# Kernel optimization log

Hardware: AMD Instinct MI355X
Metric: run time of the kernel (lower is better)

Reference implementation:

```python
import jax, jax.numpy as jnp
from jax import lax
import numpy as np

SEQ_LEN, BATCH, HIDDEN, VOCAB = 256, 32, 512, 1024


def setup_inputs() -> dict:
    key = jax.random.key(0)
    k1, k2, k3, k4, k5 = jax.random.split(key, 5)
    enc_outs = jax.random.normal(k1, (SEQ_LEN, BATCH, HIDDEN), dtype=jnp.float32)
    W = jax.random.normal(k2, (VOCAB, HIDDEN), dtype=jnp.float32) * (1.0 / np.sqrt(HIDDEN))
    b = jnp.zeros((VOCAB,), dtype=jnp.float32)
    transition = jax.random.normal(k3, (VOCAB, VOCAB), dtype=jnp.float32) * 0.05
    targets = jax.random.randint(k4, (SEQ_LEN, BATCH), 0, VOCAB, dtype=jnp.int32)
    lengths = jax.random.randint(k5, (BATCH,), 1, SEQ_LEN + 1, dtype=jnp.int32)
    return {"enc_outs": enc_outs, "W": W, "b": b, "transition": transition,
            "targets": targets, "lengths": lengths}


def _crf_loss(enc_outs, W, b, transition, targets, lengths):
    # logits: [T, B, V]
    logits = jnp.einsum('tbh,vh->tbv', enc_outs, W) + b
    T, B, V = logits.shape
    # mask[t, b] = 1 if t < lengths[b]
    mask = (jnp.arange(T)[:, None] < lengths[None, :]).astype(logits.dtype)  # [T, B]

    # ---- partition function: forward algorithm as a scan over time ----
    def step(Z, inp):
        logit_t, mask_t = inp  # [B, V], [B]
        # scores[b, i, j] = Z[b, i] + transition[i, j] + emit[b, j]
        Z_t = jax.nn.logsumexp(Z[:, :, None] + transition[None, :, :] + logit_t[:, None, :], axis=1)
        Z = jnp.where(mask_t[:, None] > 0, Z_t, Z)
        return Z, None

    Z0 = logits[0]  # [B, V]
    Z, _ = lax.scan(step, Z0, (logits[1:], mask[1:]))
    log_Z = jax.nn.logsumexp(Z, axis=1)  # [B]

    # ---- gold path score ----
    emit = jnp.take_along_axis(logits, targets[:, :, None].astype(jnp.int32), axis=2)[:, :, 0]  # [T, B]
    emit_score = jnp.sum(emit * mask, axis=0)  # [B]
    trans = transition[targets[:-1], targets[1:]]  # [T-1, B]
    trans_score = jnp.sum(trans * mask[1:], axis=0)  # [B]
    score = emit_score + trans_score

    return jnp.mean(log_Z - score)


def reference(enc_outs, W, b, transition, targets, lengths):
    return _crf_loss(enc_outs, W, b, transition, targets, lengths)
```

## Files before the change

### kernel.cpp

```cpp
#include <hip/hip_runtime.h>
#include <math.h>
#include <stdint.h>

#define TLEN 256
#define NB   32
#define HID  512
#define VOC  1024

typedef __attribute__((ext_vector_type(2))) _Float16 half2_t;
typedef __attribute__((ext_vector_type(2))) __fp16  pk16_t;
typedef __attribute__((ext_vector_type(8))) _Float16 v8h;
typedef __attribute__((ext_vector_type(4))) float    v4f;

__device__ __forceinline__ float zload(const float* p) {
    return __hip_atomic_load(p, __ATOMIC_RELAXED, __HIP_MEMORY_SCOPE_AGENT);
}
__device__ __forceinline__ float2 zload2(const float* p) {
    unsigned long long u = __hip_atomic_load((const unsigned long long*)p,
                                             __ATOMIC_RELAXED, __HIP_MEMORY_SCOPE_AGENT);
    union { unsigned long long u; float2 f; } c; c.u = u; return c.f;
}
__device__ __forceinline__ void zstore(float* p, float v) {
    __hip_atomic_store(p, v, __ATOMIC_RELAXED, __HIP_MEMORY_SCOPE_AGENT);
}
__device__ __forceinline__ uint32_t pack_pkrtz(float a, float b) {
    pk16_t h = __builtin_amdgcn_cvt_pkrtz(a, b);
    return __builtin_bit_cast(uint32_t, h);
}
__device__ __forceinline__ int udot4(uint32_t a, uint32_t b, int acc) {
#if __has_builtin(__builtin_amdgcn_udot4)
    return __builtin_amdgcn_udot4(a, b, acc, false);
#else
    return acc + (int)((a & 255u) * (b & 255u))
               + (int)(((a >> 8) & 255u) * ((b >> 8) & 255u))
               + (int)(((a >> 16) & 255u) * ((b >> 16) & 255u))
               + (int)((a >> 24) * (b >> 24));
#endif
}

__global__ __launch_bounds__(256) void gemm_mfma(
    const float* __restrict__ A, const float* __restrict__ W,
    const float* __restrict__ bias, float* __restrict__ C)
{
    const int K = HID, N = VOC;
    __shared__ _Float16 As[128][40];
    __shared__ _Float16 Ws[128][40];
    int tid  = threadIdx.x;
    int wv   = tid >> 6;
    int lane = tid & 63;
    int wy = wv >> 1, wx = wv & 1;
    int quad = lane >> 4, l16 = lane & 15;
    int row0 = blockIdx.y << 7;
    int col0 = blockIdx.x << 7;

    v4f acc[4][4] = {};

    int sr = tid >> 1;
    int sk = (tid & 1) << 4;
    const float* ap = A + (size_t)(row0 + sr) * K + sk;
    const float* wp = W + (size_t)(col0 + sr) * K + sk;

    float4 a0 = *(const float4*)(ap);
    float4 a1 = *(const float4*)(ap + 4);
    float4 a2 = *(const float4*)(ap + 8);
    float4 a3 = *(const float4*)(ap + 12);
    float4 w0 = *(const float4*)(wp);
    float4 w1 = *(const float4*)(wp + 4);
    float4 w2 = *(const float4*)(wp + 8);
    float4 w3 = *(const float4*)(wp + 12);

    for (int k0 = 0; k0 < K; k0 += 32) {
        __syncthreads();
        uint32_t* ad = (uint32_t*)&As[sr][sk];
        ad[0] = pack_pkrtz(a0.x, a0.y); ad[1] = pack_pkrtz(a0.z, a0.w);
        ad[2] = pack_pkrtz(a1.x, a1.y); ad[3] = pack_pkrtz(a1.z, a1.w);
        ad[4] = pack_pkrtz(a2.x, a2.y); ad[5] = pack_pkrtz(a2.z, a2.w);
        ad[6] = pack_pkrtz(a3.x, a3.y); ad[7] = pack_pkrtz(a3.z, a3.w);
        uint32_t* wd = (uint32_t*)&Ws[sr][sk];
        wd[0] = pack_pkrtz(w0.x, w0.y); wd[1] = pack_pkrtz(w0.z, w0.w);
        wd[2] = pack_pkrtz(w1.x, w1.y); wd[3] = pack_pkrtz(w1.z, w1.w);
        wd[4] = pack_pkrtz(w2.x, w2.y); wd[5] = pack_pkrtz(w2.z, w2.w);
        wd[6] = pack_pkrtz(w3.x, w3.y); wd[7] = pack_pkrtz(w3.z, w3.w);
        __syncthreads();
        if (k0 + 32 < K) {
            const float* apn = ap + k0 + 32;
            const float* wpn = wp + k0 + 32;
            a0 = *(const float4*)(apn);
            a1 = *(const float4*)(apn + 4);
            a2 = *(const float4*)(apn + 8);
            a3 = *(const float4*)(apn + 12);
            w0 = *(const float4*)(wpn);
            w1 = *(const float4*)(wpn + 4);
            w2 = *(const float4*)(wpn + 8);
            w3 = *(const float4*)(wpn + 12);
        }
        v8h af[4], bf[4];
        #pragma unroll
        for (int i = 0; i < 4; ++i)
            af[i] = *(const v8h*)&As[wy * 64 + i * 16 + l16][quad * 8];
        #pragma unroll
        for (int j = 0; j < 4; ++j)
            bf[j] = *(const v8h*)&Ws[wx * 64 + j * 16 + l16][quad * 8];
        #pragma unroll
        for (int i = 0; i < 4; ++i)
            #pragma unroll
            for (int j = 0; j < 4; ++j)
                acc[i][j] = __builtin_amdgcn_mfma_f32_16x16x32_f16(af[i], bf[j], acc[i][j], 0, 0, 0);
    }
    #pragma unroll
    for (int i = 0; i < 4; ++i) {
        #pragma unroll
        for (int j = 0; j < 4; ++j) {
            int ccol = col0 + wx * 64 + j * 16 + l16;
            float bb = bias[ccol];
            #pragma unroll
            for (int r = 0; r < 4; ++r) {
                int rrow = row0 + wy * 64 + i * 16 + quad * 4 + r;
                C[(size_t)rrow * N + ccol] = acc[i][j][r] + bb;
            }
        }
    }
}

__global__ __launch_bounds__(512) void crf_scan(
    const float* __restrict__ logits, float* __restrict__ Za, float* __restrict__ Zb,
    const float* __restrict__ trans, const int* __restrict__ lengths,
    unsigned int* __restrict__ cnt)
{
    __shared__ float Sred[8][64][3];
    __shared__ float Mred[8][2];
    int tid  = threadIdx.x;
    int w    = tid >> 6;
    int lane = tid & 63;
    int h    = lane >> 5;
    int li   = lane & 31;
    int bg   = blockIdx.x;
    int cc   = blockIdx.y;
    int b0   = bg * 2;

    int len2[2];
    len2[0] = lengths[b0];
    len2[1] = lengths[b0 + 1];
    int lmax = max(len2[0], len2[1]);

    int c = (cc << 6) + lane;

    uint32_t Ereg[32];
    {
        const float* tc = trans + c;
        #pragma unroll
        for (int j = 0; j < 32; ++j) {
            int v0 = (w << 7) + (j << 2);
            float e0 = __expf(tc[(size_t)(v0 + 0) << 10]) * 196.f;
            float e1 = __expf(tc[(size_t)(v0 + 1) << 10]) * 196.f;
            float e2 = __expf(tc[(size_t)(v0 + 2) << 10]) * 196.f;
            float e3 = __expf(tc[(size_t)(v0 + 3) << 10]) * 196.f;
            uint32_t q0 = (uint32_t)__float2uint_rn(fminf(e0, 255.f));
            uint32_t q1 = (uint32_t)__float2uint_rn(fminf(e1, 255.f));
            uint32_t q2 = (uint32_t)__float2uint_rn(fminf(e2, 255.f));
            uint32_t q3 = (uint32_t)__float2uint_rn(fminf(e3, 255.f));
            Ereg[j] = q0 | (q1 << 8) | (q2 << 16) | (q3 << 24);
        }
    }

    float finv = 0.f;
    if (tid < 128) {
        int b = b0 + w;
        finv = (1 < len2[w]) ? logits[(size_t)NB * VOC + (size_t)b * VOC + c]
                             : logits[(size_t)b * VOC + c];
    }

    unsigned int* cbg = &cnt[bg << 4];

    const float* src = logits;
    for (int t = 1; t < TLEN; ++t) {
        float* dst = (t & 1) ? Za : Zb;
        if (t >= lmax) {
            if (src != Za && tid < 128) {
                int b = b0 + w;
                Za[(size_t)b * VOC + c] = zload(&src[(size_t)b * VOC + c]);
            }
            return;
        }
        const float* zp = src + (size_t)(b0 + h) * VOC + (w << 7) + (li << 2);
        float2 za = zload2(zp);
        float2 zb = zload2(zp + 2);
        float m = fmaxf(fmaxf(za.x, za.y), fmaxf(zb.x, zb.y));
        #pragma unroll
        for (int off = 16; off; off >>= 1) m = fmaxf(m, __shfl_xor(m, off));
        if (li == 0) Mred[w][h] = m;
        uint32_t q0 = (uint32_t)__float2uint_rn(__expf(za.x - m) * 255.f);
        uint32_t q1 = (uint32_t)__float2uint_rn(__expf(za.y - m) * 255.f);
        uint32_t q2 = (uint32_t)__float2uint_rn(__expf(zb.x - m) * 255.f);
        uint32_t q3 = (uint32_t)__float2uint_rn(__expf(zb.y - m) * 255.f);
        uint32_t pp = q0 | (q1 << 8) | (q2 << 16) | (q3 << 24);

        int a0a = 0, a0b = 0, a1a = 0, a1b = 0;
        #pragma unroll
        for (int j = 0; j < 32; j += 2) {
            uint32_t s00 = (uint32_t)__builtin_amdgcn_readlane((int)pp, j);
            uint32_t s10 = (uint32_t)__builtin_amdgcn_readlane((int)pp, j + 32);
            uint32_t s01 = (uint32_t)__builtin_amdgcn_readlane((int)pp, j + 1);
            uint32_t s11 = (uint32_t)__builtin_amdgcn_readlane((int)pp, j + 33);
            a0a = udot4(Ereg[j], s00, a0a);
            a1a = udot4(Ereg[j], s10, a1a);
            a0b = udot4(Ereg[j + 1], s01, a0b);
            a1b = udot4(Ereg[j + 1], s11, a1b);
        }
        Sred[w][lane][0] = (float)(a0a + a0b);
        Sred[w][lane][1] = (float)(a1a + a1b);
        __syncthreads();

        if (tid < 128) {
            float M = Mred[0][w];
            #pragma unroll
            for (int ww = 1; ww < 8; ++ww) M = fmaxf(M, Mred[ww][w]);
            float S = 0.f;
            #pragma unroll
            for (int ww = 0; ww < 8; ++ww)
                S += __expf(Mred[ww][w] - M) * Sred[ww][lane][w];
            int b = b0 + w;
            float outv;
            if (t < len2[w]) outv = finv + M + __logf(S * (1.0f / (255.f * 196.f)));
            else             outv = finv;
            zstore(&dst[(size_t)b * VOC + c], outv);
            int tn = t + 1;
            if (tn < len2[w]) finv = logits[((size_t)tn * NB + b) * VOC + c];
            else              finv = outv;
        }

        __syncthreads();
        if (tid == 0) {
            unsigned int tgt = (unsigned int)(t << 4);
            unsigned int old = __hip_atomic_fetch_add(cbg, 1u, __ATOMIC_RELAXED,
                                                      __HIP_MEMORY_SCOPE_AGENT);
            if (old + 1u != tgt) {
                while (__hip_atomic_load(cbg, __ATOMIC_RELAXED,
                                         __HIP_MEMORY_SCOPE_AGENT) < tgt)
                    __builtin_amdgcn_s_sleep(1);
            }
        }
        __syncthreads();
        src = dst;
    }
}

__global__ __launch_bounds__(256) void crf_finish2(
    const float* __restrict__ Zfin, const float* __restrict__ logits,
    const float* __restrict__ trans, const int* __restrict__ targets,
    const int* __restrict__ lengths, float* __restrict__ out)
{
    __shared__ float redm[4], reds[4], reda[4];
    int b = blockIdx.x;
    int tid = threadIdx.x;
    int lane = tid & 63, wv = tid >> 6;
    const float* zr = Zfin + (size_t)b * VOC;

    float m = -1e30f;
    #pragma unroll
    for (int i = 0; i < 4; ++i) m = fmaxf(m, zr[tid + (i << 8)]);
    #pragma unroll
    for (int off = 32; off; off >>= 1) m = fmaxf(m, __shfl_xor(m, off));
    if (lane == 0) redm[wv] = m;
    __syncthreads();
    m = fmaxf(fmaxf(redm[0], redm[1]), fmaxf(redm[2], redm[3]));

    float s = 0.f;
    #pragma unroll
    for (int i = 0; i < 4; ++i) s += __expf(zr[tid + (i << 8)] - m);
    #pragma unroll
    for (int off = 32; off; off >>= 1) s += __shfl_xor(s, off);
    if (lane == 0) reds[wv] = s;

    int len = lengths[b];
    float acc = 0.f;
    int t = tid;
    if (t < len) {
        int tg = targets[t * NB + b];
        acc = logits[((size_t)t * NB + b) * VOC + tg];
        if (t >= 1) acc += trans[(size_t)targets[(t - 1) * NB + b] * VOC + tg];
    }
    #pragma unroll
    for (int off = 32; off; off >>= 1) acc += __shfl_xor(acc, off);
    if (lane == 0) reda[wv] = acc;
    __syncthreads();

    if (tid == 0) {
        float S = reds[0] + reds[1] + reds[2] + reds[3];
        float logZ = m + __logf(S);
        float score = reda[0] + reda[1] + reda[2] + reda[3];
        atomicAdd(out, (logZ - score) * (1.0f / NB));
    }
}

extern "C" void kernel_launch(void* const* d_in, const int* in_sizes, int n_in,
                              void* d_out, int out_size, void* d_ws, size_t ws_size,
                              hipStream_t stream)
{
    const float* enc   = (const float*)d_in[0];
    const float* W     = (const float*)d_in[1];
    const float* bias  = (const float*)d_in[2];
    const float* trans = (const float*)d_in[3];
    const int* targets = (const int*)d_in[4];
    const int* lengths = (const int*)d_in[5];
    float* out = (float*)d_out;

    float* ws     = (float*)d_ws;
    float* logits = ws;
    float* Za     = logits + (size_t)TLEN * NB * VOC;
    float* Zb     = Za + (size_t)NB * VOC;
    unsigned int* cnt = (unsigned int*)(Zb + (size_t)NB * VOC);

    (void)hipMemsetAsync(cnt, 0, 16 * 16 * sizeof(unsigned int), stream);
    (void)hipMemsetAsync(out, 0, sizeof(float), stream);
    gemm_mfma<<<dim3(VOC / 128, TLEN * NB / 128), 256, 0, stream>>>(enc, W, bias, logits);
    crf_scan<<<dim3(16, 16), 512, 0, stream>>>(logits, Za, Zb, trans, lengths, cnt);
    crf_finish2<<<NB, 256, 0, stream>>>(Za, logits, trans, targets, lengths, out);
}
```

Before: 606.6 us.

## Replace per-step global counter barrier with tagged data flags in scan

Removes the per-timestep atomic counter barrier across the 16 column blocks of each batch pair. Instead, each block embeds a step tag in the low 4 mantissa bits of every stored Z value and spins until the values it reads carry the expected tag. Shared reduction buffers are double-buffered by step parity, which lets the second __syncthreads per step go away. Final Z values are written to a separate Zfin buffer at each sequence's last step. The cost is lost low mantissa precision, polling on the data itself, and a memset of the Z buffers at launch.

```diff
diff --git a/kernel.cpp b/kernel.cpp
--- a/kernel.cpp
+++ b/kernel.cpp
@@ -7,14 +7,10 @@
 #define HID  512
 #define VOC  1024
 
-typedef __attribute__((ext_vector_type(2))) _Float16 half2_t;
 typedef __attribute__((ext_vector_type(2))) __fp16  pk16_t;
 typedef __attribute__((ext_vector_type(8))) _Float16 v8h;
 typedef __attribute__((ext_vector_type(4))) float    v4f;
 
-__device__ __forceinline__ float zload(const float* p) {
-    return __hip_atomic_load(p, __ATOMIC_RELAXED, __HIP_MEMORY_SCOPE_AGENT);
-}
 __device__ __forceinline__ float2 zload2(const float* p) {
     unsigned long long u = __hip_atomic_load((const unsigned long long*)p,
                                              __ATOMIC_RELAXED, __HIP_MEMORY_SCOPE_AGENT);
@@ -124,11 +120,11 @@
 
 __global__ __launch_bounds__(512) void crf_scan(
     const float* __restrict__ logits, float* __restrict__ Za, float* __restrict__ Zb,
-    const float* __restrict__ trans, const int* __restrict__ lengths,
-    unsigned int* __restrict__ cnt)
+    float* __restrict__ Zfin,
+    const float* __restrict__ trans, const int* __restrict__ lengths)
 {
-    __shared__ float Sred[8][64][3];
-    __shared__ float Mred[8][2];
+    __shared__ float Sred[2][8][64][3];
+    __shared__ float Mred[2][8][2];
     int tid  = threadIdx.x;
     int w    = tid >> 6;
     int lane = tid & 63;
@@ -166,33 +162,48 @@
     float finv = 0.f;
     if (tid < 128) {
         int b = b0 + w;
-        finv = (1 < len2[w]) ? logits[(size_t)NB * VOC + (size_t)b * VOC + c]
-                             : logits[(size_t)b * VOC + c];
-    }
-
-    unsigned int* cbg = &cnt[bg << 4];
-
-    const float* src = logits;
-    for (int t = 1; t < TLEN; ++t) {
-        float* dst = (t & 1) ? Za : Zb;
-        if (t >= lmax) {
-            if (src != Za && tid < 128) {
-                int b = b0 + w;
-                Za[(size_t)b * VOC + c] = zload(&src[(size_t)b * VOC + c]);
+        if (len2[w] == 1) {
+            Zfin[(size_t)b * VOC + c] = logits[(size_t)b * VOC + c];
+        } else {
+            finv = logits[(size_t)NB * VOC + (size_t)b * VOC + c];
+        }
+    }
+
+    float2 zlo = {0.f, 0.f}, zhi = {0.f, 0.f};
+    const int lenH = len2[h];
+    const size_t zoff = (size_t)(b0 + h) * VOC + (size_t)((w << 7) + (li << 2));
+
+    for (int t = 1; t < lmax; ++t) {
+        int par = t & 1;
+        if (t == 1) {
+            const float* zp = logits + zoff;
+            zlo = *(const float2*)zp;
+            zhi = *(const float2*)(zp + 2);
+        } else if (t - 1 < lenH) {
+            const float* zp = ((t & 1) ? Zb : Za) + zoff;
+            unsigned tg = 8u | (unsigned)((t - 1) & 7);
+            for (;;) {
+                float2 a = zload2(zp);
+                float2 b = zload2(zp + 2);
+                unsigned x0 = __builtin_bit_cast(unsigned, a.x) & 15u;
+                unsigned x1 = __builtin_bit_cast(unsigned, a.y) & 15u;
+                unsigned x2 = __builtin_bit_cast(unsigned, b.x) & 15u;
+                unsigned x3 = __builtin_bit_cast(unsigned, b.y) & 15u;
+                if (((x0 ^ tg) | (x1 ^ tg) | (x2 ^ tg) | (x3 ^ tg)) == 0u) {
+                    zlo = a; zhi = b; break;
+                }
+                __builtin_amdgcn_s_sleep(1);
             }
-            return;
-        }
-        const float* zp = src + (size_t)(b0 + h) * VOC + (w << 7) + (li << 2);
-        float2 za = zload2(zp);
-        float2 zb = zload2(zp + 2);
-        float m = fmaxf(fmaxf(za.x, za.y), fmaxf(zb.x, zb.y));
+        }
+
+        float m = fmaxf(fmaxf(zlo.x, zlo.y), fmaxf(zhi.x, zhi.y));
         #pragma unroll
         for (int off = 16; off; off >>= 1) m = fmaxf(m, __shfl_xor(m, off));
-        if (li == 0) Mred[w][h] = m;
-        uint32_t q0 = (uint32_t)__float2uint_rn(__expf(za.x - m) * 255.f);
-        uint32_t q1 = (uint32_t)__float2uint_rn(__expf(za.y - m) * 255.f);
-        uint32_t q2 = (uint32_t)__float2uint_rn(__expf(zb.x - m) * 255.f);
-        uint32_t q3 = (uint32_t)__float2uint_rn(__expf(zb.y - m) * 255.f);
+        if (li == 0) Mred[par][w][h] = m;
+        uint32_t q0 = (uint32_t)__float2uint_rn(__expf(zlo.x - m) * 255.f);
+        uint32_t q1 = (uint32_t)__float2uint_rn(__expf(zlo.y - m) * 255.f);
+        uint32_t q2 = (uint32_t)__float2uint_rn(__expf(zhi.x - m) * 255.f);
+        uint32_t q3 = (uint32_t)__float2uint_rn(__expf(zhi.y - m) * 255.f);
         uint32_t pp = q0 | (q1 << 8) | (q2 << 16) | (q3 << 24);
 
         int a0a = 0, a0b = 0, a1a = 0, a1b = 0;
@@ -207,41 +218,33 @@
             a0b = udot4(Ereg[j + 1], s01, a0b);
             a1b = udot4(Ereg[j + 1], s11, a1b);
         }
-        Sred[w][lane][0] = (float)(a0a + a0b);
-        Sred[w][lane][1] = (float)(a1a + a1b);
+        Sred[par][w][lane][0] = (float)(a0a + a0b);
+        Sred[par][w][lane][1] = (float)(a1a + a1b);
         __syncthreads();
 
         if (tid < 128) {
-            float M = Mred[0][w];
+            float M = Mred[par][0][w];
             #pragma unroll
-            for (int ww = 1; ww < 8; ++ww) M = fmaxf(M, Mred[ww][w]);
+            for (int ww = 1; ww < 8; ++ww) M = fmaxf(M, Mred[par][ww][w]);
             float S = 0.f;
             #pragma unroll
             for (int ww = 0; ww < 8; ++ww)
-                S += __expf(Mred[ww][w] - M) * Sred[ww][lane][w];
+                S += __expf(Mred[par][ww][w] - M) * Sred[par][ww][lane][w];
             int b = b0 + w;
-            float outv;
-            if (t < len2[w]) outv = finv + M + __logf(S * (1.0f / (255.f * 196.f)));
-            else             outv = finv;
-            zstore(&dst[(size_t)b * VOC + c], outv);
-            int tn = t + 1;
-            if (tn < len2[w]) finv = logits[((size_t)tn * NB + b) * VOC + c];
-            else              finv = outv;
-        }
-
-        __syncthreads();
-        if (tid == 0) {
-            unsigned int tgt = (unsigned int)(t << 4);
-            unsigned int old = __hip_atomic_fetch_add(cbg, 1u, __ATOMIC_RELAXED,
-                                                      __HIP_MEMORY_SCOPE_AGENT);
-            if (old + 1u != tgt) {
-                while (__hip_atomic_load(cbg, __ATOMIC_RELAXED,
-                                         __HIP_MEMORY_SCOPE_AGENT) < tgt)
-                    __builtin_amdgcn_s_sleep(1);
+            int lenW = len2[w];
+            if (t < lenW) {
+                float outv = finv + M + __logf(S * (1.0f / (255.f * 196.f)));
+                float* dst = (t & 1) ? Za : Zb;
+                unsigned ub = (__builtin_bit_cast(unsigned, outv) & ~15u)
+                            | 8u | (unsigned)(t & 7);
+                zstore(&dst[(size_t)b * VOC + c], __builtin_bit_cast(float, ub));
+                if (t == lenW - 1) {
+                    Zfin[(size_t)b * VOC + c] = outv;
+                } else {
+                    finv = logits[((size_t)(t + 1) * NB + b) * VOC + c];
+                }
             }
         }
-        __syncthreads();
-        src = dst;
     }
 }
 
@@ -309,11 +312,11 @@
     float* logits = ws;
     float* Za     = logits + (size_t)TLEN * NB * VOC;
     float* Zb     = Za + (size_t)NB * VOC;
-    unsigned int* cnt = (unsigned int*)(Zb + (size_t)NB * VOC);
-
-    (void)hipMemsetAsync(cnt, 0, 16 * 16 * sizeof(unsigned int), stream);
+    float* Zfin   = Zb + (size_t)NB * VOC;
+
+    (void)hipMemsetAsync(Za, 0, 2 * (size_t)NB * VOC * sizeof(float), stream);
     (void)hipMemsetAsync(out, 0, sizeof(float), stream);
     gemm_mfma<<<dim3(VOC / 128, TLEN * NB / 128), 256, 0, stream>>>(enc, W, bias, logits);
-    crf_scan<<<dim3(16, 16), 512, 0, stream>>>(logits, Za, Zb, trans, lengths, cnt);
-    crf_finish2<<<NB, 256, 0, stream>>>(Za, logits, trans, targets, lengths, out);
-}
+    crf_scan<<<dim3(16, 16), 512, 0, stream>>>(logits, Za, Zb, Zfin, trans, lengths);
+    crf_finish2<<<NB, 256, 0, stream>>>(Zfin, logits, trans, targets, lengths, out);
+}
```

Result: no change. 615.8 us (+1.5%).
